# Performance work log

Measured on AMD Instinct MI355X. Metric: run time of the kernel, lower is better.

## Reference

```python
import jax, jax.numpy as jnp
import numpy as np
import math

D_MODEL = 1024
NHEAD = 16
D_HEAD = D_MODEL // NHEAD
B, S = 2, 2048


def setup_inputs() -> dict:
    key = jax.random.key(0)
    ks = jax.random.split(key, 8)
    scale = 1.0 / math.sqrt(D_MODEL)
    return {
        "q": jax.random.normal(ks[0], (B, S, D_MODEL), jnp.float32),
        "k": jax.random.normal(ks[1], (B, S, D_MODEL), jnp.float32),
        "v": jax.random.normal(ks[2], (B, S, D_MODEL), jnp.float32),
        "mask": jax.random.randint(ks[3], (B, S, S), 0, 2) == 1,
        "w_q": jax.random.normal(ks[4], (D_MODEL, D_MODEL), jnp.float32) * scale,
        "w_k": jax.random.normal(ks[5], (D_MODEL, D_MODEL), jnp.float32) * scale,
        "w_v": jax.random.normal(ks[6], (D_MODEL, D_MODEL), jnp.float32) * scale,
        "w_o": jax.random.normal(ks[7], (D_MODEL, D_MODEL), jnp.float32) * scale,
    }


def reference(q, k, v, mask, w_q, w_k, w_v, w_o):
    # Linear layers (torch Linear: x @ W.T), then the module's view(B, H, -1, d_head),
    # which is a plain reshape (sequence gets folded with heads), NOT a head-transpose.
    qh = (q @ w_q.T).reshape(B, NHEAD, -1, D_HEAD)  # (B,H,S,dh) via raw reshape
    kh = (k @ w_k.T).reshape(B, NHEAD, -1, D_HEAD)
    vh = (v @ w_v.T).reshape(B, NHEAD, -1, D_HEAD)

    u = jnp.einsum("bhqd,bhkd->bhqk", qh, kh) / math.sqrt(D_HEAD)  # (B,H,S,S)
    m = mask[:, None]  # (B,1,S,S)
    u = jnp.where(m, -jnp.inf, u)
    attn = jax.nn.softmax(u, axis=-1)
    attn = jnp.where(m, 0.0, attn)
    out = jnp.einsum("bhqk,bhkd->bhqd", attn, vh)  # (B,H,S,dh)
    out = out.reshape(B, -1, D_MODEL)  # raw reshape back, matching the module
    return out @ w_o.T
```

## Files before the change

kernel.cpp:

```cpp
#include <hip/hip_runtime.h>
#include <hip/hip_bf16.h>
#include <stdint.h>


typedef __attribute__((ext_vector_type(8))) short short8;
typedef __attribute__((ext_vector_type(4))) short s4v;
typedef __attribute__((ext_vector_type(4))) float floatx4;
using bf16 = __hip_bfloat16;

#define QSCALE 0.18033688011112042f

#define MFMA16(a, b, c) __builtin_amdgcn_mfma_f32_16x16x32_bf16(a, b, c, 0, 0, 0)

__device__ __forceinline__ void load_lds16(const bf16* g, bf16* l) {
  __builtin_amdgcn_global_load_lds(
      (const __attribute__((address_space(1))) void*)g,
      (__attribute__((address_space(3))) void*)l, 16, 0, 0);
}

__device__ __forceinline__ float scrub(float x) {
  return (x == x && fabsf(x) < 1e30f) ? x : 0.0f;
}

__device__ __forceinline__ int swz64(int row, int col) {
  return row * 64 + (col ^ ((row & 7) << 3));
}
__device__ __forceinline__ int swz128(int row, int col) {
  return row * 128 + (col ^ ((row & 15) << 3));
}

__global__ void k_detect(const uint16_t* __restrict__ q,
                         const uint16_t* __restrict__ mask,
                         int* __restrict__ flags) {
  __shared__ int f32, cat;
  const int tid = threadIdx.x;
  if (tid == 0) { f32 = 0; cat = 0; }
  __syncthreads();
  int hit = 0;
#pragma unroll
  for (int j = 0; j < 8; j++) {
    const short8 v8 = *(const short8*)(q + ((size_t)tid * 8 + j) * 8);
#pragma unroll
    for (int t = 0; t < 8; t++) {
      const int e = (((unsigned short)v8[t]) >> 7) & 0xFF;
      if (e == 0 || e == 0xFF) hit = 1;
    }
  }
  if (hit) atomicOr(&f32, 1);
  int c = 0;
  {
    const short8 m8 = *(const short8*)(mask + (size_t)tid * 8);
#pragma unroll
    for (int t = 0; t < 8; t++) {
      const uint32_t hw = (unsigned short)m8[t];
      const int i = tid * 8 + t;
      if (hw == 0x3C00u) c |= 4;
      else if (hw == 0x3F80u) c |= (i & 1) ? 2 : 1;
      else if (hw > 1u) c |= 8;
    }
  }
  if (c) atomicOr(&cat, c);
  __syncthreads();
  if (tid == 0) {
    flags[0] = f32;
    const int cc = cat;
    int mode;
    if (cc & 4)      mode = 2;
    else if (cc & 1) mode = 2;
    else if (cc & 2) mode = 3;
    else if (cc & 8) mode = 0;
    else             mode = 1;
    flags[1] = mode;
  }
}

__global__ __launch_bounds__(256) void k_prep(
    const void* __restrict__ qf, const void* __restrict__ kf,
    const void* __restrict__ vf, const void* __restrict__ wqf,
    const void* __restrict__ wkf, const void* __restrict__ wvf,
    const void* __restrict__ wof, const void* __restrict__ maskp,
    bf16* __restrict__ dst, uint32_t* __restrict__ bits, int conv) {
  __shared__ int sf32, scat;
  const int tid = threadIdx.x;
  if (tid == 0) { sf32 = 0; scat = 0; }
  __syncthreads();
  {
    int hit = 0;
    const uint16_t* qh = (const uint16_t*)qf;
#pragma unroll
    for (int j = 0; j < 8; j++) {
      const short8 v8 = *(const short8*)(qh + ((size_t)tid * 8 + j) * 8);
#pragma unroll
      for (int t = 0; t < 8; t++) {
        const int e = (((unsigned short)v8[t]) >> 7) & 0xFF;
        if (e == 0 || e == 0xFF) hit = 1;
      }
    }
    if (hit) atomicOr(&sf32, 1);
    int c = 0;
    const short8 m8 = *(const short8*)((const uint16_t*)maskp + (size_t)tid * 8);
#pragma unroll
    for (int t = 0; t < 8; t++) {
      const uint32_t hw = (unsigned short)m8[t];
      const int i = tid * 8 + t;
      if (hw == 0x3C00u) c |= 4;
      else if (hw == 0x3F80u) c |= (i & 1) ? 2 : 1;
      else if (hw > 1u) c |= 8;
    }
    if (c) atomicOr(&scat, c);
  }
  __syncthreads();
  const int f32 = sf32;
  int mmode;
  {
    const int cc = scat;
    if (cc & 4)      mmode = 2;
    else if (cc & 1) mmode = 2;
    else if (cc & 2) mmode = 3;
    else if (cc & 8) mmode = 0;
    else             mmode = 1;
  }
  const size_t t0 = (size_t)blockIdx.x * 256 + tid;
  const size_t nthr = (size_t)gridDim.x * 256;
  if (conv) {
    for (size_t c = t0; c < 2097152; c += nthr) {
      const size_t e = c * 8;
      const void* src; size_t off; float sc = 1.0f;
      if (e < 4194304)       { src = qf;  off = e;            sc = QSCALE; }
      else if (e < 8388608)  { src = kf;  off = e - 4194304;  }
      else if (e < 12582912) { src = vf;  off = e - 8388608;  }
      else if (e < 13631488) { src = wqf; off = e - 12582912; }
      else if (e < 14680064) { src = wkf; off = e - 13631488; }
      else if (e < 15728640) { src = wvf; off = e - 14680064; }
      else                   { src = wof; off = e - 15728640; }
      union { short8 v8; bf16 b[8]; } u;
      if (f32) {
        const float4* s4 = (const float4*)src + (off >> 2);
        const float4 f0 = s4[0];
        const float4 f1 = s4[1];
        u.b[0] = __float2bfloat16(f0.x * sc); u.b[1] = __float2bfloat16(f0.y * sc);
        u.b[2] = __float2bfloat16(f0.z * sc); u.b[3] = __float2bfloat16(f0.w * sc);
        u.b[4] = __float2bfloat16(f1.x * sc); u.b[5] = __float2bfloat16(f1.y * sc);
        u.b[6] = __float2bfloat16(f1.z * sc); u.b[7] = __float2bfloat16(f1.w * sc);
      } else {
        u.v8 = *(const short8*)((const bf16*)src + off);
        if (sc != 1.0f) {
#pragma unroll
          for (int j = 0; j < 8; j++)
            u.b[j] = __float2bfloat16(__bfloat162float(u.b[j]) * sc);
        }
      }
      *(short8*)(dst + e) = u.v8;
    }
  }
  const int wid = (int)(t0 >> 6), ln = (int)(t0 & 63);
  const int nw = (int)(nthr >> 6);
  const int NG = 2 * 2048 * 2048 / 64;
  for (int g = wid; g < NG; g += nw) {
    const size_t e = (size_t)g * 64 + ln;
    bool v;
    if (mmode == 1)      v = ((const int*)maskp)[e] != 0;
    else if (mmode == 0) v = ((const uint8_t*)maskp)[e] != 0;
    else if (mmode == 2) v = ((const uint16_t*)maskp)[e] != 0;
    else                 v = ((const uint32_t*)maskp)[e] != 0;
    const unsigned long long m = __ballot(v);
    if (ln == 0)       bits[(size_t)g * 2]     = (uint32_t)m;
    else if (ln == 32) bits[(size_t)g * 2 + 1] = (uint32_t)(m >> 32);
  }
}

template <int ROWS>
__device__ __forceinline__ void stage_b16(const bf16* __restrict__ src,
                                          bf16* __restrict__ dst,
                                          int wv, int ln) {
#pragma unroll
  for (int i = 0; i < ROWS / 32; i++) {
    const int seg = i * 4 + wv;
    const int row = seg * 8 + (ln >> 3);
    const int ch = ln & 7;
    load_lds16(src + (size_t)row * 1024 + ((ch ^ (row & 7)) << 3),
               dst + seg * 512);
  }
}

template <int ROWS>
__device__ __forceinline__ void stage_f32(const float* __restrict__ src,
                                          bf16* __restrict__ dst, int tid) {
#pragma unroll
  for (int it = 0; it < ROWS / 32; ++it) {
    const int e0 = (it * 256 + tid) * 8;
    const int row = e0 >> 6, col = e0 & 63;
    const float* s = src + (size_t)row * 1024 + col;
    const float4 f0 = *(const float4*)s;
    const float4 f1 = *(const float4*)(s + 4);
    union { short8 v; bf16 b[8]; } u;
    u.b[0] = __float2bfloat16(f0.x); u.b[1] = __float2bfloat16(f0.y);
    u.b[2] = __float2bfloat16(f0.z); u.b[3] = __float2bfloat16(f0.w);
    u.b[4] = __float2bfloat16(f1.x); u.b[5] = __float2bfloat16(f1.y);
    u.b[6] = __float2bfloat16(f1.z); u.b[7] = __float2bfloat16(f1.w);
    *(short8*)(dst + swz64(row, col)) = u.v;
  }
}

template <int MT>
__device__ __forceinline__ void gemm_t(const void* __restrict__ A, int a_f32,
                                       const void* __restrict__ W, int w_f32,
                                       bf16* __restrict__ Out,
                                       float* __restrict__ OutF, int mode,
                                       float oscale) {
  constexpr int TI = MT / 32;
  __shared__ bf16 As[MT * 64];
  __shared__ bf16 Bs[128 * 64];
  const int tid = threadIdx.x;
  const int wv = tid >> 6, ln = tid & 63;
  const int g = ln >> 4;
  const int m0 = blockIdx.x * MT, n0 = blockIdx.y * 128;
  const int wm = (wv >> 1) * (MT / 2), wn = (wv & 1) * 64;
  floatx4 acc[TI][4] = {};
  for (int k0 = 0; k0 < 1024; k0 += 64) {
    __syncthreads();
    if (a_f32) stage_f32<MT>((const float*)A + (size_t)m0 * 1024 + k0, As, tid);
    else       stage_b16<MT>((const bf16*)A + (size_t)m0 * 1024 + k0, As, wv, ln);
    if (w_f32) stage_f32<128>((const float*)W + (size_t)n0 * 1024 + k0, Bs, tid);
    else       stage_b16<128>((const bf16*)W + (size_t)n0 * 1024 + k0, Bs, wv, ln);
    __syncthreads();
    const short* Ap = (const short*)As;
    const short* Bp = (const short*)Bs;
    short8 af[TI][2], bfr[4][2];
#pragma unroll
    for (int t = 0; t < TI; t++)
#pragma unroll
      for (int kc = 0; kc < 2; kc++)
        af[t][kc] = *(const short8*)(Ap + swz64(wm + t * 16 + (ln & 15), kc * 32 + g * 8));
#pragma unroll
    for (int t = 0; t < 4; t++)
#pragma unroll
      for (int kc = 0; kc < 2; kc++)
        bfr[t][kc] = *(const short8*)(Bp + swz64(wn + t * 16 + (ln & 15), kc * 32 + g * 8));
#pragma unroll
    for (int kc = 0; kc < 2; kc++)
#pragma unroll
      for (int ti = 0; ti < TI; ti++)
#pragma unroll
        for (int tj = 0; tj < 4; tj++)
          acc[ti][tj] = MFMA16(af[ti][kc], bfr[tj][kc], acc[ti][tj]);
  }
#pragma unroll
  for (int ti = 0; ti < TI; ti++)
#pragma unroll
    for (int tj = 0; tj < 4; tj++)
#pragma unroll
      for (int r = 0; r < 4; r++) {
        const int m = m0 + wm + ti * 16 + (ln >> 4) * 4 + r;
        const int n = n0 + wn + tj * 16 + (ln & 15);
        if (mode == 2) {
          OutF[(size_t)m * 1024 + n] = scrub(acc[ti][tj][r]);
        } else {
          const int b = m >> 11, s = m & 2047;
          const int h = s >> 7, sl = s & 127;
          const int oc = n >> 6, d = n & 63;
          const int t = sl * 16 + oc;
          size_t idx;
          if (mode == 0) idx = ((size_t)(b * 16 + h) * 2048 + t) * 64 + d;
          else           idx = ((size_t)(b * 16 + h) * 64 + d) * 2048 + t;
          Out[idx] = __float2bfloat16(scrub(acc[ti][tj][r]) * oscale);
        }
      }
}

__global__ __launch_bounds__(256, 2) void k_proj(
    const void* __restrict__ q, const void* __restrict__ k, const void* __restrict__ v,
    const void* __restrict__ wq, const void* __restrict__ wk, const void* __restrict__ wvv,
    bf16* __restrict__ QH, bf16* __restrict__ KH, bf16* __restrict__ VT,
    const int* __restrict__ flags, int conv) {
  const int z = blockIdx.z;
  const int fl = conv ? 0 : flags[0];
  const void* A = (z == 0) ? q : (z == 1) ? k : v;
  const void* W = (z == 0) ? wq : (z == 1) ? wk : wvv;
  bf16* O = (z == 0) ? QH : (z == 1) ? KH : VT;
  const float osc = (z == 0 && !conv) ? QSCALE : 1.0f;
  gemm_t<128>(A, fl, W, fl, O, nullptr, (z == 2) ? 1 : 0, osc);
}

__global__ __launch_bounds__(256, 2) void k_outp(
    const bf16* __restrict__ A, const void* __restrict__ W,
    float* __restrict__ Out, const int* __restrict__ flags, int conv) {
  const int wf = conv ? 0 : flags[0];
  gemm_t<64>(A, 0, W, wf, nullptr, Out, 2, 1.0f);
}

__global__ __launch_bounds__(512, 4) void k_attn(
    const bf16* __restrict__ QH, const bf16* __restrict__ KH,
    const bf16* __restrict__ VT, const uint32_t* __restrict__ bits,
    bf16* __restrict__ OB) {
  constexpr int S = 2048, D = 64;
  constexpr float NEGB = -60000.0f;
  __shared__ bf16 Ks[128 * 64];
  __shared__ bf16 Vs[64 * 128];
  __shared__ bf16 Ps[128 * 128];
  const int tid = threadIdx.x, wv = tid >> 6, ln = tid & 63;
  const int g = ln >> 4, lq = ln & 15;
  const int flat = blockIdx.y * gridDim.x + blockIdx.x;
  const int xcd = flat & 7, ii = flat >> 3;
  const int bh = (xcd << 2) | (ii >> 4);
  const int q0 = (ii & 15) * 128;
  const int b = bh >> 4, h = bh & 15;
  const int qrow = wv * 16;

  short8 qf[2];
#pragma unroll
  for (int kc = 0; kc < 2; kc++) {
    const int qr = q0 + qrow + lq;
    qf[kc] = *(const short8*)(QH + ((size_t)bh * S + qr) * D + kc * 32 + g * 8);
  }

  const bf16* Kbase = KH + (size_t)bh * S * D;
  const bf16* Vbase = VT + (size_t)bh * D * S;
  const uint32_t* Mb = bits + (size_t)b * 131072 + (size_t)(q0 + qrow + lq) * 64;
  short8 kreg[2], vreg[2];

#define LOAD_KV(kt_)                                                     \
  {                                                                      \
    const bf16* Kg = Kbase + (size_t)(kt_) * 128 * D;                    \
    const bf16* Vg = Vbase + (kt_) * 128;                                \
    _Pragma("unroll")                                                    \
    for (int i = 0; i < 2; i++) {                                        \
      const int seg = i * 8 + wv;                                        \
      const int e = seg * 512 + ln * 8;                                  \
      kreg[i] = *(const short8*)(Kg + e);                                \
      const int fb = (seg * 64 + ln) * 16;                               \
      const int dd = fb >> 8, cb = (fb & 255) >> 1;                      \
      vreg[i] = *(const short8*)(Vg + (size_t)dd * S + cb);              \
    }                                                                    \
  }

#define STORE_KV()                                                       \
  {                                                                      \
    _Pragma("unroll")                                                    \
    for (int i = 0; i < 2; i++) {                                        \
      const int seg = i * 8 + wv;                                        \
      const int e = seg * 512 + ln * 8;                                  \
      *(short8*)(Ks + swz64(e >> 6, e & 63)) = kreg[i];                  \
      const int fb = (seg * 64 + ln) * 16;                               \
      const int dd = fb >> 8, cb = (fb & 255) >> 1;                      \
      *(short8*)(Vs + swz128(dd, cb)) = vreg[i];                         \
    }                                                                    \
  }

  float lacc0 = 0.f, lacc1 = 0.f;
  floatx4 oacc[4] = {};

  LOAD_KV(0);
  uint4 mvn = *(const uint4*)(Mb + 0);
  STORE_KV();
  __syncthreads();

  for (int kt = 0; kt < 16; kt++) {
    const uint4 mv = mvn;
    if (kt < 15) {
      LOAD_KV(kt + 1);
      mvn = *(const uint4*)(Mb + (kt + 1) * 4);
    }

    floatx4 sc[8];
    {
      const short* Kp = (const short*)Ks;
      __builtin_amdgcn_s_setprio(1);
#pragma unroll
      for (int tj = 0; tj < 8; tj++) {
        const int krow = tj * 16 + lq;
        const int kcol = g * 8;
        const short8 k0f = *(const short8*)(Kp + swz64(krow, kcol));
        const short8 k1f = *(const short8*)(Kp + swz64(krow, 32 + kcol));
        floatx4 z = {0.f, 0.f, 0.f, 0.f};
        z = MFMA16(k0f, qf[0], z);
        z = MFMA16(k1f, qf[1], z);
        sc[tj] = z;
      }
      __builtin_amdgcn_s_setprio(0);
    }

    {
      const int prow = qrow + lq;
      const uint32_t mw4[4] = {mv.x, mv.y, mv.z, mv.w};
#pragma unroll
      for (int tj = 0; tj < 8; tj++) {
        const uint32_t nib = mw4[tj >> 1] >> (((tj & 1) << 4) + (g << 2));
        uint32_t pw0, pw1;
        {
          float p0, p1, p2, p3;
          const float u0 = (nib & 1u) ? NEGB : sc[tj][0];
          const float u1 = (nib & 2u) ? NEGB : sc[tj][1];
          const float u2 = (nib & 4u) ? NEGB : sc[tj][2];
          const float u3 = (nib & 8u) ? NEGB : sc[tj][3];
          asm("v_exp_f32 %0, %1" : "=v"(p0) : "v"(u0));
          asm("v_exp_f32 %0, %1" : "=v"(p1) : "v"(u1));
          asm("v_exp_f32 %0, %1" : "=v"(p2) : "v"(u2));
          asm("v_exp_f32 %0, %1" : "=v"(p3) : "v"(u3));
          lacc0 += p0 + p2;
          lacc1 += p1 + p3;
          asm("v_cvt_pk_bf16_f32 %0, %1, %2" : "=v"(pw0) : "v"(p0), "v"(p1));
          asm("v_cvt_pk_bf16_f32 %0, %1, %2" : "=v"(pw1) : "v"(p2), "v"(p3));
        }
        uint2 pu; pu.x = pw0; pu.y = pw1;
        *(uint2*)(Ps + swz128(prow, tj * 16 + g * 4)) = pu;
      }
    }

    {
      const short* Pp = (const short*)Ps;
      const short* Vp = (const short*)Vs;
      __builtin_amdgcn_s_setprio(1);
#pragma unroll
      for (int kc = 0; kc < 4; kc++) {
        const short8 ap = *(const short8*)(Pp + swz128(qrow + lq, kc * 32 + g * 8));
#pragma unroll
        for (int tj = 0; tj < 4; tj++) {
          const short8 bv = *(const short8*)(Vp + swz128(tj * 16 + lq, kc * 32 + g * 8));
          oacc[tj] = MFMA16(ap, bv, oacc[tj]);
        }
      }
      __builtin_amdgcn_s_setprio(0);
    }
    __syncthreads();
    if (kt < 15) STORE_KV();
    __syncthreads();
  }

  {
    float s2 = lacc0 + lacc1;
    s2 += __shfl_xor(s2, 16);
    s2 += __shfl_xor(s2, 32);
    const float rlq = (s2 > 1e-35f) ? 1.f / s2 : 0.f;
    bf16* row = Ps + wv * 2048;
#pragma unroll
    for (int r = 0; r < 4; r++) {
      const float rl = __shfl(rlq, (ln & 48) | ((g << 2) + r), 64);
#pragma unroll
      for (int tj = 0; tj < 4; tj++) {
        row[(g * 4 + r) * 64 + tj * 16 + lq] =
            __float2bfloat16(scrub(oacc[tj][r] * rl));
      }
    }
    __builtin_amdgcn_s_waitcnt(0);
    const int s = h * 128 + ((q0 + qrow) >> 4);
    bf16* Og = OB + ((size_t)b * S + s) * 1024;
#pragma unroll
    for (int c = 0; c < 2; c++)
      *(short8*)(Og + c * 512 + ln * 8) = *(const short8*)(row + c * 512 + ln * 8);
  }
#undef LOAD_KV
#undef STORE_KV
}

extern "C" void kernel_launch(void* const* d_in, const int* in_sizes, int n_in,
                              void* d_out, int out_size, void* d_ws, size_t ws_size,
                              hipStream_t stream) {
  const void* q  = d_in[0];
  const void* k  = d_in[1];
  const void* v  = d_in[2];
  const void* mask = d_in[3];
  const void* wq = d_in[4];
  const void* wk = d_in[5];
  const void* wv = d_in[6];
  const void* wo = d_in[7];
  float* out = (float*)d_out;

  char* ws = (char*)d_ws;
  int* flags = (int*)ws;
  bf16* QH = (bf16*)(ws + 256);
  bf16* KH = QH + 4194304;
  bf16* VT = KH + 4194304;
  uint32_t* bits = (uint32_t*)(VT + 4194304);
  bf16* CV = (bf16*)(ws + 256 + 3 * 8388608 + 1048576);

  const size_t NEED = 256 + 3 * 8388608 + 1048576 + 33554432;
  const int conv = (ws_size >= NEED) ? 1 : 0;

  k_prep<<<2048, 256, 0, stream>>>(q, k, v, wq, wk, wv, wo, mask, CV, bits, conv);
  if (!conv)
    k_detect<<<1, 256, 0, stream>>>((const uint16_t*)q, (const uint16_t*)mask, flags);

  const void *pq = q, *pk = k, *pv = v, *pwq = wq, *pwk = wk, *pwv = wv, *pwo = wo;
  if (conv) {
    pq  = CV;             pk  = CV + 4194304;  pv  = CV + 8388608;
    pwq = CV + 12582912;  pwk = CV + 13631488; pwv = CV + 14680064;
    pwo = CV + 15728640;
  }

  k_proj<<<dim3(32, 8, 3), 256, 0, stream>>>(pq, pk, pv, pwq, pwk, pwv,
                                             QH, KH, VT, flags, conv);
  k_attn<<<dim3(16, 32), 512, 0, stream>>>(QH, KH, VT, bits, QH );
  k_outp<<<dim3(64, 8), 256, 0, stream>>>(QH, pwo, out, flags, conv);
}
```

Baseline: 264.2 us.

## Double-buffer K/V in attention, split P into halves, remap GEMM blocks per XCD

The attention kernel now keeps two K/V buffers in LDS. The next tile is stored into the spare buffer, so only one barrier per iteration is needed instead of two. Softmax and the P·V product are split into two 64-column halves, which halves the P scratch buffer and interleaves exp work with MFMA. The projection and output GEMM kernels remap their flat block index so that neighbouring tiles sharing A/W rows land on the same XCD, aiming for better L2 reuse. Total LDS use in attention grows, which may affect occupancy.

```diff
diff --git a/kernel.cpp b/kernel.cpp
--- a/kernel.cpp
+++ b/kernel.cpp
@@ -207,14 +207,13 @@
                                        const void* __restrict__ W, int w_f32,
                                        bf16* __restrict__ Out,
                                        float* __restrict__ OutF, int mode,
-                                       float oscale) {
+                                       float oscale, int m0, int n0) {
   constexpr int TI = MT / 32;
   __shared__ bf16 As[MT * 64];
   __shared__ bf16 Bs[128 * 64];
   const int tid = threadIdx.x;
   const int wv = tid >> 6, ln = tid & 63;
   const int g = ln >> 4;
-  const int m0 = blockIdx.x * MT, n0 = blockIdx.y * 128;
   const int wm = (wv >> 1) * (MT / 2), wn = (wv & 1) * 64;
   floatx4 acc[TI][4] = {};
   for (int k0 = 0; k0 < 1024; k0 += 64) {
@@ -273,20 +272,29 @@
     const void* __restrict__ wq, const void* __restrict__ wk, const void* __restrict__ wvv,
     bf16* __restrict__ QH, bf16* __restrict__ KH, bf16* __restrict__ VT,
     const int* __restrict__ flags, int conv) {
-  const int z = blockIdx.z;
+  const int flat = blockIdx.x + (blockIdx.y << 5) + (blockIdx.z << 8);
+  const int xcd = flat & 7, j = flat >> 3;
+  const int x = (xcd << 2) | (j & 3);
+  const int rem = j >> 2;
+  const int y = rem & 7, z = rem >> 3;
   const int fl = conv ? 0 : flags[0];
   const void* A = (z == 0) ? q : (z == 1) ? k : v;
   const void* W = (z == 0) ? wq : (z == 1) ? wk : wvv;
   bf16* O = (z == 0) ? QH : (z == 1) ? KH : VT;
   const float osc = (z == 0 && !conv) ? QSCALE : 1.0f;
-  gemm_t<128>(A, fl, W, fl, O, nullptr, (z == 2) ? 1 : 0, osc);
+  gemm_t<128>(A, fl, W, fl, O, nullptr, (z == 2) ? 1 : 0, osc, x * 128, y * 128);
 }
 
 __global__ __launch_bounds__(256, 2) void k_outp(
     const bf16* __restrict__ A, const void* __restrict__ W,
     float* __restrict__ Out, const int* __restrict__ flags, int conv) {
+  const int flat = blockIdx.x + (blockIdx.y << 6);
+  const int xcd = flat & 7, j = flat >> 3;
+  const int bh = (xcd << 2) | ((j & 7) >> 1);
+  const int x = ((bh >> 4) << 5) + ((bh & 15) << 1) + (j & 1);
+  const int y = j >> 3;
   const int wf = conv ? 0 : flags[0];
-  gemm_t<64>(A, 0, W, wf, nullptr, Out, 2, 1.0f);
+  gemm_t<64>(A, 0, W, wf, nullptr, Out, 2, 1.0f, x * 64, y * 128);
 }
 
 __global__ __launch_bounds__(512, 4) void k_attn(
@@ -295,9 +303,9 @@
     bf16* __restrict__ OB) {
   constexpr int S = 2048, D = 64;
   constexpr float NEGB = -60000.0f;
-  __shared__ bf16 Ks[128 * 64];
-  __shared__ bf16 Vs[64 * 128];
-  __shared__ bf16 Ps[128 * 128];
+  __shared__ bf16 Ks[2 * 128 * 64];
+  __shared__ bf16 Vs[2 * 64 * 128];
+  __shared__ bf16 Ps[128 * 64];
   const int tid = threadIdx.x, wv = tid >> 6, ln = tid & 63;
   const int g = ln >> 4, lq = ln & 15;
   const int flat = blockIdx.y * gridDim.x + blockIdx.x;
@@ -334,16 +342,18 @@
     }                                                                    \
   }
 
-#define STORE_KV()                                                       \
+#define STORE_KV(buf_)                                                   \
   {                                                                      \
+    bf16* Kd = Ks + (buf_) * 8192;                                       \
+    bf16* Vd = Vs + (buf_) * 8192;                                       \
     _Pragma("unroll")                                                    \
     for (int i = 0; i < 2; i++) {                                        \
       const int seg = i * 8 + wv;                                        \
       const int e = seg * 512 + ln * 8;                                  \
-      *(short8*)(Ks + swz64(e >> 6, e & 63)) = kreg[i];                  \
+      *(short8*)(Kd + swz64(e >> 6, e & 63)) = kreg[i];                  \
       const int fb = (seg * 64 + ln) * 16;                               \
       const int dd = fb >> 8, cb = (fb & 255) >> 1;                      \
-      *(short8*)(Vs + swz128(dd, cb)) = vreg[i];                         \
+      *(short8*)(Vd + swz128(dd, cb)) = vreg[i];                         \
     }                                                                    \
   }
 
@@ -352,10 +362,11 @@
 
   LOAD_KV(0);
   uint4 mvn = *(const uint4*)(Mb + 0);
-  STORE_KV();
+  STORE_KV(0);
   __syncthreads();
 
   for (int kt = 0; kt < 16; kt++) {
+    const int cur = kt & 1;
     const uint4 mv = mvn;
     if (kt < 15) {
       LOAD_KV(kt + 1);
@@ -364,7 +375,7 @@
 
     floatx4 sc[8];
     {
-      const short* Kp = (const short*)Ks;
+      const short* Kp = (const short*)(Ks + cur * 8192);
       __builtin_amdgcn_s_setprio(1);
 #pragma unroll
       for (int tj = 0; tj < 8; tj++) {
@@ -383,48 +394,52 @@
     {
       const int prow = qrow + lq;
       const uint32_t mw4[4] = {mv.x, mv.y, mv.z, mv.w};
-#pragma unroll
-      for (int tj = 0; tj < 8; tj++) {
-        const uint32_t nib = mw4[tj >> 1] >> (((tj & 1) << 4) + (g << 2));
-        uint32_t pw0, pw1;
-        {
-          float p0, p1, p2, p3;
-          const float u0 = (nib & 1u) ? NEGB : sc[tj][0];
-          const float u1 = (nib & 2u) ? NEGB : sc[tj][1];
-          const float u2 = (nib & 4u) ? NEGB : sc[tj][2];
-          const float u3 = (nib & 8u) ? NEGB : sc[tj][3];
-          asm("v_exp_f32 %0, %1" : "=v"(p0) : "v"(u0));
-          asm("v_exp_f32 %0, %1" : "=v"(p1) : "v"(u1));
-          asm("v_exp_f32 %0, %1" : "=v"(p2) : "v"(u2));
-          asm("v_exp_f32 %0, %1" : "=v"(p3) : "v"(u3));
-          lacc0 += p0 + p2;
-          lacc1 += p1 + p3;
-          asm("v_cvt_pk_bf16_f32 %0, %1, %2" : "=v"(pw0) : "v"(p0), "v"(p1));
-          asm("v_cvt_pk_bf16_f32 %0, %1, %2" : "=v"(pw1) : "v"(p2), "v"(p3));
+      const short* Vp = (const short*)(Vs + cur * 8192);
+#pragma unroll
+      for (int hf = 0; hf < 2; hf++) {
+#pragma unroll
+        for (int t4 = 0; t4 < 4; t4++) {
+          const int tj = hf * 4 + t4;
+          const uint32_t nib = mw4[tj >> 1] >> (((tj & 1) << 4) + (g << 2));
+          uint32_t pw0, pw1;
+          {
+            float p0, p1, p2, p3;
+            const float u0 = (nib & 1u) ? NEGB : sc[tj][0];
+            const float u1 = (nib & 2u) ? NEGB : sc[tj][1];
+            const float u2 = (nib & 4u) ? NEGB : sc[tj][2];
+            const float u3 = (nib & 8u) ? NEGB : sc[tj][3];
+            asm("v_exp_f32 %0, %1" : "=v"(p0) : "v"(u0));
+            asm("v_exp_f32 %0, %1" : "=v"(p1) : "v"(u1));
+            asm("v_exp_f32 %0, %1" : "=v"(p2) : "v"(u2));
+            asm("v_exp_f32 %0, %1" : "=v"(p3) : "v"(u3));
+            lacc0 += p0 + p2;
+            lacc1 += p1 + p3;
+            asm("v_cvt_pk_bf16_f32 %0, %1, %2" : "=v"(pw0) : "v"(p0), "v"(p1));
+            asm("v_cvt_pk_bf16_f32 %0, %1, %2" : "=v"(pw1) : "v"(p2), "v"(p3));
+          }
+          uint2 pu; pu.x = pw0; pu.y = pw1;
+          *(uint2*)(Ps + swz64(prow, t4 * 16 + g * 4)) = pu;
         }
-        uint2 pu; pu.x = pw0; pu.y = pw1;
-        *(uint2*)(Ps + swz128(prow, tj * 16 + g * 4)) = pu;
+        const short* Pp = (const short*)Ps;
+        __builtin_amdgcn_s_setprio(1);
+#pragma unroll
+        for (int kc = 0; kc < 2; kc++) {
+          const short8 ap = *(const short8*)(Pp + swz64(prow, kc * 32 + g * 8));
+#pragma unroll
+          for (int tj = 0; tj < 4; tj++) {
+            const short8 bv = *(const short8*)(
+                Vp + swz128(tj * 16 + lq, (hf * 2 + kc) * 32 + g * 8));
+            oacc[tj] = MFMA16(ap, bv, oacc[tj]);
+          }
+        }
+        __builtin_amdgcn_s_setprio(0);
       }
     }
 
-    {
-      const short* Pp = (const short*)Ps;
-      const short* Vp = (const short*)Vs;
-      __builtin_amdgcn_s_setprio(1);
-#pragma unroll
-      for (int kc = 0; kc < 4; kc++) {
-        const short8 ap = *(const short8*)(Pp + swz128(qrow + lq, kc * 32 + g * 8));
-#pragma unroll
-        for (int tj = 0; tj < 4; tj++) {
-          const short8 bv = *(const short8*)(Vp + swz128(tj * 16 + lq, kc * 32 + g * 8));
-          oacc[tj] = MFMA16(ap, bv, oacc[tj]);
-        }
-      }
-      __builtin_amdgcn_s_setprio(0);
-    }
-    __syncthreads();
-    if (kt < 15) STORE_KV();
-    __syncthreads();
+    if (kt < 15) {
+      STORE_KV(cur ^ 1);
+      __syncthreads();
+    }
   }
 
   {
@@ -432,7 +447,7 @@
     s2 += __shfl_xor(s2, 16);
     s2 += __shfl_xor(s2, 32);
     const float rlq = (s2 > 1e-35f) ? 1.f / s2 : 0.f;
-    bf16* row = Ps + wv * 2048;
+    bf16* row = Ps + wv * 1024;
 #pragma unroll
     for (int r = 0; r < 4; r++) {
       const float rl = __shfl(rlq, (ln & 48) | ((g << 2) + r), 64);
```

Result: slower. 270.1 us (+2.2%).
